# Performance work log

Measured on AMD Instinct MI355X. Metric: run time of the kernel, lower is better.

## Reference

```python
import jax, jax.numpy as jnp
import numpy as np

N_NODES = 100000
N_EDGES = 1600000
N_GRAPHS = 256
D_IN = 128
D_HID = 128
D_OUT = 64


def graph_conv(x, src, dst, W_rel, b_rel, W_root):
    # PyG GraphConv: out = lin_rel(mean_{j->i} x_j) + lin_root(x)
    msgs = jax.ops.segment_sum(x[src], dst, num_segments=N_NODES)  # [N, d]
    deg = jax.ops.segment_sum(jnp.ones((src.shape[0],), x.dtype), dst, num_segments=N_NODES)
    agg = msgs / jnp.maximum(deg, 1.0)[:, None]
    return agg @ W_rel + b_rel + x @ W_root


def setup_inputs() -> dict:
    key = jax.random.key(0)
    ks = jax.random.split(key, 12)
    x = jax.random.normal(ks[0], (N_NODES, D_IN), dtype=jnp.float32)
    edge_index = jax.random.randint(ks[1], (2, N_EDGES), 0, N_NODES, dtype=jnp.int64)
    batch = jnp.sort(jax.random.randint(ks[2], (N_NODES,), 0, N_GRAPHS, dtype=jnp.int64))
    def lin(k, fan_in, fan_out):
        bound = 1.0 / np.sqrt(fan_in)
        return jax.random.uniform(k, (fan_in, fan_out), jnp.float32, -bound, bound)
    inp = {
        "x": x, "edge_index": edge_index, "batch": batch,
        "W1_rel": lin(ks[3], D_IN, D_HID), "b1_rel": jnp.zeros((D_HID,), jnp.float32), "W1_root": lin(ks[4], D_IN, D_HID),
        "W2_rel": lin(ks[5], D_HID, D_HID), "b2_rel": jnp.zeros((D_HID,), jnp.float32), "W2_root": lin(ks[6], D_HID, D_HID),
        "W3_rel": lin(ks[7], D_HID, D_HID), "b3_rel": jnp.zeros((D_HID,), jnp.float32), "W3_root": lin(ks[8], D_HID, D_HID),
        "Wl": lin(ks[9], D_HID, D_OUT), "bl": jnp.zeros((D_OUT,), jnp.float32),
    }
    return inp


def reference(x, edge_index, batch, W1_rel, b1_rel, W1_root, W2_rel, b2_rel, W2_root,
              W3_rel, b3_rel, W3_root, Wl, bl):
    src, dst = edge_index[0], edge_index[1]
    h = jax.nn.relu(graph_conv(x, src, dst, W1_rel, b1_rel, W1_root))
    h = jax.nn.relu(graph_conv(h, src, dst, W2_rel, b2_rel, W2_root))
    h = graph_conv(h, src, dst, W3_rel, b3_rel, W3_root)
    # global mean pool over graphs
    sums = jax.ops.segment_sum(h, batch, num_segments=N_GRAPHS)          # [G, d]
    cnts = jax.ops.segment_sum(jnp.ones((h.shape[0],), h.dtype), batch, num_segments=N_GRAPHS)
    pooled = sums / jnp.maximum(cnts, 1.0)[:, None]
    # dropout is identity at inference
    return pooled @ Wl + bl  # [G, D_OUT]
```

## Files before the change

### kernel.cpp

```cpp
#include <hip/hip_runtime.h>
#include <hip/hip_bf16.h>

#define N_NODES  100000
#define N_EDGES  1600000
#define N_GRAPHS 256
#define DCH      128
#define DOUT     64
#define NB       391
#define PADB     512
#define SLACK    4608
#define CHUNK    2048
#define NBINA    782

typedef short v8s __attribute__((ext_vector_type(8)));
typedef float v4f __attribute__((ext_vector_type(4)));

static __device__ __forceinline__ float bf2f(unsigned short u) {
    unsigned int x = ((unsigned int)u) << 16;
    return __builtin_bit_cast(float, x);
}
static __device__ __forceinline__ unsigned short f2bf(float f) {
    unsigned int x = __builtin_bit_cast(unsigned int, f);
    unsigned int r = (x + 0x7fffu + ((x >> 16) & 1u)) >> 16;
    return (unsigned short)r;
}
static __device__ __forceinline__ int clampi(int v, int lo, int hi) {
    return v < lo ? lo : (v > hi ? hi : v);
}

__global__ void __launch_bounds__(256) binA_kernel(const int* __restrict__ src, const int* __restrict__ dst,
                                                   int* __restrict__ gcur, unsigned* __restrict__ region) {
    __shared__ uint2 stage[CHUNK];
    __shared__ int hcnt[PADB], hcnt2[PADB], hoff[PADB], garr[PADB];
    __shared__ int s2[256];
    int tid = threadIdx.x;
    int e0  = blockIdx.x * CHUNK;
    int nedge = N_EDGES - e0; if (nedge > CHUNK) nedge = CHUNK;

    for (int b = tid; b < PADB; b += 256) { hcnt[b] = 0; hcnt2[b] = 0; }
    __syncthreads();

    int es[CHUNK / 256], ed[CHUNK / 256];
    #pragma unroll
    for (int j = 0; j < CHUNK / 256; j++) {
        int e = e0 + j * 256 + tid;
        if (e < N_EDGES) {
            es[j] = clampi(src[e], 0, N_NODES - 1);
            ed[j] = clampi(dst[e], 0, N_NODES - 1);
            atomicAdd(&hcnt[ed[j] >> 8], 1);
        } else { es[j] = -1; ed[j] = 0; }
    }
    __syncthreads();

    int v0 = hcnt[2 * tid], v1 = hcnt[2 * tid + 1];
    s2[tid] = v0 + v1; __syncthreads();
    for (int off = 1; off < 256; off <<= 1) {
        int xx = (tid >= off) ? s2[tid - off] : 0;
        __syncthreads();
        s2[tid] += xx;
        __syncthreads();
    }
    int excl = s2[tid] - (v0 + v1);
    hoff[2 * tid] = excl; hoff[2 * tid + 1] = excl + v0;
    __syncthreads();

    for (int b = tid; b < NB; b += 256) {
        int c = hcnt[b];
        garr[b] = b * SLACK + ((c > 0) ? atomicAdd(&gcur[b], c) : 0);
    }
    __syncthreads();

    #pragma unroll
    for (int j = 0; j < CHUNK / 256; j++) {
        if (es[j] >= 0) {
            int b = ed[j] >> 8;
            int pos = atomicAdd(&hcnt2[b], 1) + hoff[b];
            stage[pos] = (uint2){(unsigned)es[j], (unsigned)ed[j]};
        }
    }
    __syncthreads();

    for (int i = tid; i < nedge; i += 256) {
        uint2 en = stage[i];
        int b = (int)(en.y >> 8);
        int gpos = garr[b] + (i - hoff[b]);
        if (gpos < (b + 1) * SLACK)
            region[gpos] = (en.x << 8) | (en.y & 255u);
    }
}

__global__ void __launch_bounds__(256) binFinishPrep_kernel(
    const unsigned* __restrict__ region, const int* __restrict__ gcur,
    int* __restrict__ rowptr, int* __restrict__ csr,
    const float* __restrict__ x, unsigned short* __restrict__ B2,
    const float* __restrict__ W1rel, const float* __restrict__ W1root,
    const float* __restrict__ W2rel, const float* __restrict__ W2root,
    const float* __restrict__ W3rel, const float* __restrict__ W3root,
    unsigned short* __restrict__ frag,
    unsigned short* __restrict__ z1, unsigned short* __restrict__ z2)
{
    __shared__ int h[256], sc[256], cur[256], s2[256], hoff[PADB];
    int tid = threadIdx.x;

    if (blockIdx.x >= NB) {
        int bid = blockIdx.x - NB;
        if (bid < 12500) {
            size_t i = ((size_t)bid * 256 + tid) * 4;
            float4 f = *reinterpret_cast<const float4*>(x + i);
            uint2 o;
            o.x = ((unsigned)f2bf(f.y) << 16) | (unsigned)f2bf(f.x);
            o.y = ((unsigned)f2bf(f.w) << 16) | (unsigned)f2bf(f.z);
            *reinterpret_cast<uint2*>(B2 + i) = o;
        } else if (bid < 12548) {
            int gid = (bid - 12500) * 256 + tid;
            int lane = gid & 63;
            int nt   = (gid >> 6) & 7;
            int kt   = (gid >> 9) & 7;
            int L    = gid >> 12;
            const float* rel  = (L == 0) ? W1rel  : (L == 1) ? W2rel  : W3rel;
            const float* root = (L == 0) ? W1root : (L == 1) ? W2root : W3root;
            int n  = nt * 16 + (lane & 15);
            int k0 = kt * 32 + (lane >> 4) * 8;
            unsigned short o[8];
            #pragma unroll
            for (int j = 0; j < 8; j++) {
                int k = k0 + j;
                float w = (k < 128) ? rel[k * 128 + n] : root[(k - 128) * 128 + n];
                o[j] = f2bf(w);
            }
            uint4 u;
            u.x = (unsigned)o[0] | ((unsigned)o[1] << 16);
            u.y = (unsigned)o[2] | ((unsigned)o[3] << 16);
            u.z = (unsigned)o[4] | ((unsigned)o[5] << 16);
            u.w = (unsigned)o[6] | ((unsigned)o[7] << 16);
            *reinterpret_cast<uint4*>(frag + (size_t)gid * 8) = u;
        } else {
            if (tid < 64)       reinterpret_cast<unsigned*>(z1)[tid] = 0;
            else if (tid < 128) reinterpret_cast<unsigned*>(z2)[tid - 64] = 0;
        }
        return;
    }

    int b = blockIdx.x;
    int c0 = gcur[2 * tid];     if (c0 > SLACK) c0 = SLACK;
    int c1 = gcur[2 * tid + 1]; if (c1 > SLACK) c1 = SLACK;
    s2[tid] = c0 + c1;
    h[tid] = 0;
    __syncthreads();
    for (int off = 1; off < 256; off <<= 1) {
        int xx = (tid >= off) ? s2[tid - off] : 0;
        __syncthreads();
        s2[tid] += xx;
        __syncthreads();
    }
    int excl = s2[tid] - (c0 + c1);
    hoff[2 * tid] = excl; hoff[2 * tid + 1] = excl + c0;
    __syncthreads();
    if (b == 0 && tid == 255) rowptr[N_NODES] = s2[255];
    int base = hoff[b];
    int size = gcur[b]; if (size > SLACK) size = SLACK;
    int node0 = b * 256;
    for (int j = tid; j < size; j += 256) {
        unsigned loc = region[b * SLACK + j] & 255u;
        atomicAdd(&h[loc], 1);
    }
    __syncthreads();
    int v = h[tid]; sc[tid] = v; __syncthreads();
    for (int off = 1; off < 256; off <<= 1) {
        int xx = (tid >= off) ? sc[tid - off] : 0;
        __syncthreads();
        sc[tid] += xx;
        __syncthreads();
    }
    int myptr = base + sc[tid] - v;
    int node = node0 + tid;
    if (node < N_NODES) rowptr[node] = myptr;
    cur[tid] = myptr;
    __syncthreads();
    for (int j = tid; j < size; j += 256) {
        unsigned en = region[b * SLACK + j];
        unsigned loc = en & 255u;
        int p = atomicAdd(&cur[loc], 1);
        if (p >= 0 && p < N_EDGES) csr[p] = (int)(en >> 8);
    }
}

__global__ void __launch_bounds__(256, 6) layer_kernel(
    const unsigned short* __restrict__ hin,
    const int* __restrict__ rowptr, const int* __restrict__ csr,
    const unsigned short* __restrict__ frag, const float* __restrict__ bias,
    unsigned short* __restrict__ hout,
    const int* __restrict__ batch, float* __restrict__ psum, int mode)
{
    __shared__ __attribute__((aligned(16))) unsigned short As[16 * DCH];
    const int wave = threadIdx.x >> 6;
    const int lane = threadIdx.x & 63;
    const int l16  = lane & 15;
    const int quad = lane >> 4;
    const int base = blockIdx.x * 16;
    char* Asb = reinterpret_cast<char*>(As);

    #pragma unroll
    for (int k = 0; k < 4; k++) {
        const int row  = wave * 4 + k;
        const int node = base + row;
        const int r0 = rowptr[node];
        const int r1 = rowptr[node + 1];
        float a0 = 0.f, a1 = 0.f;
        int t = csr[r0 + l16];
        for (int c = r0; c < r1; c += 16) {
            int tn = csr[c + 16 + l16];
            int idx = (c + l16 < r1) ? t : N_NODES;
            #pragma unroll
            for (int j = 0; j < 16; j++) {
                int s = __builtin_amdgcn_readlane(idx, j);
                unsigned v = *reinterpret_cast<const unsigned*>(hin + (size_t)s * DCH + lane * 2);
                a0 += bf2f((unsigned short)(v & 0xffffu));
                a1 += bf2f((unsigned short)(v >> 16));
            }
            t = tn;
        }
        int deg = r1 - r0;
        float inv = 1.0f / (float)(deg > 1 ? deg : 1);
        unsigned o = ((unsigned)f2bf(a1 * inv) << 16) | (unsigned)f2bf(a0 * inv);
        *reinterpret_cast<unsigned*>(Asb + row * 256 + ((lane * 4) ^ ((row & 7) << 4))) = o;
    }
    __syncthreads();

    const int nt0 = wave * 2;
    v4f acc0 = (v4f){0.f, 0.f, 0.f, 0.f};
    v4f acc1 = (v4f){0.f, 0.f, 0.f, 0.f};
    #pragma unroll
    for (int kt = 0; kt < 8; kt++) {
        v8s av;
        if (kt < 4) {
            int co = (kt * 64 + quad * 16) ^ ((l16 & 7) << 4);
            av = *reinterpret_cast<const v8s*>(Asb + l16 * 256 + co);
        } else {
            int ak = (kt - 4) * 32 + quad * 8;
            av = *reinterpret_cast<const v8s*>(hin + (size_t)(base + l16) * DCH + ak);
        }
        v8s b0 = *reinterpret_cast<const v8s*>(frag + (((size_t)(kt * 8 + nt0)) * 64 + lane) * 8);
        v8s b1 = *reinterpret_cast<const v8s*>(frag + (((size_t)(kt * 8 + nt0 + 1)) * 64 + lane) * 8);
        acc0 = __builtin_amdgcn_mfma_f32_16x16x32_bf16(av, b0, acc0, 0, 0, 0);
        acc1 = __builtin_amdgcn_mfma_f32_16x16x32_bf16(av, b1, acc1, 0, 0, 0);
    }

    const int n0 = nt0 * 16 + l16;
    const int n1 = n0 + 16;
    const float bv0 = bias[n0];
    const float bv1 = bias[n1];

    if (mode != 2) {
        #pragma unroll
        for (int r = 0; r < 4; r++) {
            int row = base + quad * 4 + r;
            float x0 = acc0[r] + bv0;
            float x1 = acc1[r] + bv1;
            if (mode == 1) { x0 = fmaxf(x0, 0.f); x1 = fmaxf(x1, 0.f); }
            hout[(size_t)row * DCH + n0] = f2bf(x0);
            hout[(size_t)row * DCH + n1] = f2bf(x1);
        }
    } else {
        bool fast = (batch[base] == batch[base + 15]);
        if (fast) {
            int g = batch[base];
            float s0 = acc0[0] + acc0[1] + acc0[2] + acc0[3] + 4.0f * bv0;
            float s1 = acc1[0] + acc1[1] + acc1[2] + acc1[3] + 4.0f * bv1;
            s0 += __shfl_xor(s0, 16); s0 += __shfl_xor(s0, 32);
            s1 += __shfl_xor(s1, 16); s1 += __shfl_xor(s1, 32);
            if (quad == 0) {
                atomicAdd(&psum[g * DCH + n0], s0);
                atomicAdd(&psum[g * DCH + n1], s1);
            }
        } else {
            int g[4];
            #pragma unroll
            for (int r = 0; r < 4; r++) g[r] = batch[base + quad * 4 + r];
            float s0 = 0.f, s1 = 0.f; int cg = -1;
            #pragma unroll
            for (int r = 0; r < 4; r++) {
                if (g[r] != cg) {
                    if (cg >= 0) {
                        atomicAdd(&psum[cg * DCH + n0], s0);
                        atomicAdd(&psum[cg * DCH + n1], s1);
                    }
                    s0 = 0.f; s1 = 0.f; cg = g[r];
                }
                s0 += acc0[r] + bv0;
                s1 += acc1[r] + bv1;
            }
            if (cg >= 0) {
                atomicAdd(&psum[cg * DCH + n0], s0);
                atomicAdd(&psum[cg * DCH + n1], s1);
            }
        }
    }
}

static __device__ __forceinline__ int lowerb(const int* __restrict__ a, int n, int key) {
    int lo = 0, hi = n;
    while (lo < hi) { int mid = (lo + hi) >> 1; if (a[mid] < key) lo = mid + 1; else hi = mid; }
    return lo;
}

__global__ void __launch_bounds__(64) final_kernel(const float* __restrict__ psum,
                                                   const int* __restrict__ batch,
                                                   const float* __restrict__ Wl, const float* __restrict__ bl,
                                                   float* __restrict__ out) {
    __shared__ float ps[DCH];
    __shared__ int bounds[2];
    int g = blockIdx.x, tid = threadIdx.x;
    if (tid == 0) {
        bounds[0] = lowerb(batch, N_NODES, g);
        bounds[1] = lowerb(batch, N_NODES, g + 1);
    }
    __syncthreads();
    int cnt = bounds[1] - bounds[0];
    float inv = 1.0f / (float)(cnt > 1 ? cnt : 1);
    ps[tid] = psum[g * DCH + tid] * inv;
    ps[tid + 64] = psum[g * DCH + tid + 64] * inv;
    __syncthreads();
    float o = 0.f;
    #pragma unroll 4
    for (int c = 0; c < DCH; c++) o += ps[c] * Wl[c * DOUT + tid];
    out[g * DOUT + tid] = o + bl[tid];
}

extern "C" void kernel_launch(void* const* d_in, const int* in_sizes, int n_in,
                              void* d_out, int out_size, void* d_ws, size_t ws_size,
                              hipStream_t stream) {
    const float* x     = (const float*)d_in[0];
    const int*   edge  = (const int*)d_in[1];
    const int*   src   = edge;
    const int*   dst   = edge + N_EDGES;
    const int*   batch = (const int*)d_in[2];
    const float* W1rel  = (const float*)d_in[3];
    const float* b1     = (const float*)d_in[4];
    const float* W1root = (const float*)d_in[5];
    const float* W2rel  = (const float*)d_in[6];
    const float* b2     = (const float*)d_in[7];
    const float* W2root = (const float*)d_in[8];
    const float* W3rel  = (const float*)d_in[9];
    const float* b3     = (const float*)d_in[10];
    const float* W3root = (const float*)d_in[11];
    const float* Wl     = (const float*)d_in[12];
    const float* bl     = (const float*)d_in[13];
    float* out = (float*)d_out;

    char* ws = (char*)d_ws;
    size_t off = 0;
    auto carve = [&](size_t bytes) -> void* {
        void* p = ws + off;
        off += (bytes + 255) & ~(size_t)255;
        return p;
    };
    int*            rowptr  = (int*)carve((size_t)(N_NODES + 1) * 4);
    int*            csr     = (int*)carve((size_t)(N_EDGES + 64) * 4);
    int*            gcur    = (int*)carve((size_t)PADB * 4 + (size_t)N_GRAPHS * DCH * 4);
    float*          psum    = (float*)(gcur + PADB);
    unsigned short* frag    = (unsigned short*)carve((size_t)3 * 8 * 8 * 64 * 8 * 2);
    unsigned short* B1      = (unsigned short*)carve((size_t)(N_NODES + 1) * DCH * 2);
    unsigned short* B2      = (unsigned short*)carve((size_t)(N_NODES + 1) * DCH * 2);
    unsigned*       region  = (unsigned*)B1;

    hipMemsetAsync(gcur, 0, (size_t)PADB * 4 + (size_t)N_GRAPHS * DCH * 4, stream);

    binA_kernel<<<NBINA, 256, 0, stream>>>(src, dst, gcur, region);
    binFinishPrep_kernel<<<NB + 12549, 256, 0, stream>>>(region, gcur, rowptr, csr,
                                                         x, B2, W1rel, W1root, W2rel, W2root, W3rel, W3root,
                                                         frag, B1 + (size_t)N_NODES * DCH, B2 + (size_t)N_NODES * DCH);

    const int layerGrid = N_NODES / 16;

    layer_kernel<<<layerGrid, 256, 0, stream>>>(B2, rowptr, csr, frag,         b1, B1, batch, psum, 1);
    layer_kernel<<<layerGrid, 256, 0, stream>>>(B1, rowptr, csr, frag + 32768, b2, B2, batch, psum, 1);
    layer_kernel<<<layerGrid, 256, 0, stream>>>(B2, rowptr, csr, frag + 65536, b3, B1, batch, psum, 2);

    final_kernel<<<N_GRAPHS, 64, 0, stream>>>(psum, batch, Wl, bl, out);
}
```

Baseline: 381.5 us.

## Split x conversion across binning kernels and balance aggregation rows dynamically

The fp32-to-bf16 conversion of x is split in half. The first half now runs as extra blocks in the edge-binning kernel and the second half stays in the finish/prep kernel, so both launches carry independent work alongside the binning. In the layer kernel, the fixed assignment of 4 rows per wave is replaced by a shared atomic counter, letting waves pull rows dynamically and balance uneven node degrees. This adds an LDS atomic and a shuffle per row, and it loses the unrolled loop.

```diff
diff --git a/kernel.cpp b/kernel.cpp
--- a/kernel.cpp
+++ b/kernel.cpp
@@ -11,6 +11,8 @@
 #define SLACK    4608
 #define CHUNK    2048
 #define NBINA    782
+#define PREPA    6250
+#define PREPB    6250
 
 typedef short v8s __attribute__((ext_vector_type(8)));
 typedef float v4f __attribute__((ext_vector_type(4)));
@@ -28,12 +30,31 @@
     return v < lo ? lo : (v > hi ? hi : v);
 }
 
-__global__ void __launch_bounds__(256) binA_kernel(const int* __restrict__ src, const int* __restrict__ dst,
-                                                   int* __restrict__ gcur, unsigned* __restrict__ region) {
+static __device__ __forceinline__ void cvt_block(const float* __restrict__ x,
+                                                 unsigned short* __restrict__ B2, int bid, int tid) {
+    size_t i = ((size_t)bid * 256 + tid) * 4;
+    float4 f = *reinterpret_cast<const float4*>(x + i);
+    uint2 o;
+    o.x = ((unsigned)f2bf(f.y) << 16) | (unsigned)f2bf(f.x);
+    o.y = ((unsigned)f2bf(f.w) << 16) | (unsigned)f2bf(f.z);
+    *reinterpret_cast<uint2*>(B2 + i) = o;
+}
+
+__global__ void __launch_bounds__(256) binAprepA_kernel(
+    const int* __restrict__ src, const int* __restrict__ dst,
+    int* __restrict__ gcur, unsigned* __restrict__ region,
+    const float* __restrict__ x, unsigned short* __restrict__ B2)
+{
     __shared__ uint2 stage[CHUNK];
     __shared__ int hcnt[PADB], hcnt2[PADB], hoff[PADB], garr[PADB];
     __shared__ int s2[256];
     int tid = threadIdx.x;
+
+    if (blockIdx.x >= NBINA) {
+        cvt_block(x, B2, blockIdx.x - NBINA, tid);
+        return;
+    }
+
     int e0  = blockIdx.x * CHUNK;
     int nedge = N_EDGES - e0; if (nedge > CHUNK) nedge = CHUNK;
 
@@ -89,7 +110,7 @@
     }
 }
 
-__global__ void __launch_bounds__(256) binFinishPrep_kernel(
+__global__ void __launch_bounds__(256) binFinishPrepB_kernel(
     const unsigned* __restrict__ region, const int* __restrict__ gcur,
     int* __restrict__ rowptr, int* __restrict__ csr,
     const float* __restrict__ x, unsigned short* __restrict__ B2,
@@ -104,15 +125,10 @@
 
     if (blockIdx.x >= NB) {
         int bid = blockIdx.x - NB;
-        if (bid < 12500) {
-            size_t i = ((size_t)bid * 256 + tid) * 4;
-            float4 f = *reinterpret_cast<const float4*>(x + i);
-            uint2 o;
-            o.x = ((unsigned)f2bf(f.y) << 16) | (unsigned)f2bf(f.x);
-            o.y = ((unsigned)f2bf(f.w) << 16) | (unsigned)f2bf(f.z);
-            *reinterpret_cast<uint2*>(B2 + i) = o;
-        } else if (bid < 12548) {
-            int gid = (bid - 12500) * 256 + tid;
+        if (bid < PREPB) {
+            cvt_block(x, B2, PREPA + bid, tid);
+        } else if (bid < PREPB + 48) {
+            int gid = (bid - PREPB) * 256 + tid;
             int lane = gid & 63;
             int nt   = (gid >> 6) & 7;
             int kt   = (gid >> 9) & 7;
@@ -193,6 +209,7 @@
     const int* __restrict__ batch, float* __restrict__ psum, int mode)
 {
     __shared__ __attribute__((aligned(16))) unsigned short As[16 * DCH];
+    __shared__ int ctr;
     const int wave = threadIdx.x >> 6;
     const int lane = threadIdx.x & 63;
     const int l16  = lane & 15;
@@ -200,9 +217,14 @@
     const int base = blockIdx.x * 16;
     char* Asb = reinterpret_cast<char*>(As);
 
-    #pragma unroll
-    for (int k = 0; k < 4; k++) {
-        const int row  = wave * 4 + k;
+    if (threadIdx.x == 0) ctr = 0;
+    __syncthreads();
+
+    for (;;) {
+        int row;
+        if (lane == 0) row = atomicAdd(&ctr, 1);
+        row = __shfl(row, 0);
+        if (row >= 16) break;
         const int node = base + row;
         const int r0 = rowptr[node];
         const int r1 = rowptr[node + 1];
@@ -366,10 +388,10 @@
 
     hipMemsetAsync(gcur, 0, (size_t)PADB * 4 + (size_t)N_GRAPHS * DCH * 4, stream);
 
-    binA_kernel<<<NBINA, 256, 0, stream>>>(src, dst, gcur, region);
-    binFinishPrep_kernel<<<NB + 12549, 256, 0, stream>>>(region, gcur, rowptr, csr,
-                                                         x, B2, W1rel, W1root, W2rel, W2root, W3rel, W3root,
-                                                         frag, B1 + (size_t)N_NODES * DCH, B2 + (size_t)N_NODES * DCH);
+    binAprepA_kernel<<<NBINA + PREPA, 256, 0, stream>>>(src, dst, gcur, region, x, B2);
+    binFinishPrepB_kernel<<<NB + PREPB + 49, 256, 0, stream>>>(region, gcur, rowptr, csr,
+                                                               x, B2, W1rel, W1root, W2rel, W2root, W3rel, W3root,
+                                                               frag, B1 + (size_t)N_NODES * DCH, B2 + (size_t)N_NODES * DCH);
 
     const int layerGrid = N_NODES / 16;
 
```

Result: no change. 383.6 us (+0.6%).
